# Kernel optimization log

Hardware: AMD Instinct MI355X
Metric: run time of the kernel (lower is better)

## Reference

```python
import jax, jax.numpy as jnp
import numpy as np

E = 768   # embed_size
H = 64    # head_embed_size
B = 8
T = 4096  # == ctx_size


def setup_inputs() -> dict:
    key = jax.random.key(0)
    k1, k2, k3, k4 = jax.random.split(key, 4)
    inputs = jax.random.normal(k1, (B, T, E), dtype=jnp.float32)
    # Linear weights stored as (E, H) so projection is x @ W
    scale = 1.0 / np.sqrt(E)
    Wq = jax.random.uniform(k2, (E, H), dtype=jnp.float32, minval=-scale, maxval=scale)
    Wk = jax.random.uniform(k3, (E, H), dtype=jnp.float32, minval=-scale, maxval=scale)
    Wv = jax.random.uniform(k4, (E, H), dtype=jnp.float32, minval=-scale, maxval=scale)
    return {"inputs": inputs, "Wq": Wq, "Wk": Wk, "Wv": Wv}


def reference(inputs, Wq, Wk, Wv):
    Tlen = inputs.shape[1]
    q = inputs @ Wq  # (B,T,H)
    k = inputs @ Wk  # (B,T,H)
    v = inputs @ Wv  # (B,T,H)
    # NOTE: original module does NOT scale by 1/sqrt(H) — faithful reproduction.
    scores = jnp.einsum('bqh,bkh->bqk', q, k)  # (B,T,T)
    causal = jnp.tril(jnp.ones((Tlen, Tlen), dtype=bool))
    scores = jnp.where(causal, scores, -jnp.inf)
    attn = jax.nn.softmax(scores, axis=-1)
    # dropout=0 -> identity
    out = jnp.einsum('bqk,bkh->bqh', attn, v)  # (B,T,H)
    return out
```

## Files before the change

### kernel.cpp

```cpp
#include <hip/hip_runtime.h>
#include <hip/hip_bf16.h>

#define E_DIM 768
#define H_DIM 64
#define B_SZ 8
#define T_SZ 4096
#define BT (B_SZ * T_SZ)

typedef __attribute__((ext_vector_type(8))) short short8;
typedef __attribute__((ext_vector_type(4))) short bf16x4;
typedef __attribute__((ext_vector_type(4))) float floatx4;

#define RAWBAR() __asm__ volatile("s_waitcnt lgkmcnt(0)\n\ts_barrier" ::: "memory")

static __device__ __forceinline__ unsigned short bf1(float a) {
    __hip_bfloat16 h = __float2bfloat16(a);
    unsigned short u; __builtin_memcpy(&u, &h, 2); return u;
}
static __device__ __forceinline__ unsigned int pk2(float a, float b) {
    __hip_bfloat162 h = __float22bfloat162_rn(float2{a, b});
    unsigned int u; __builtin_memcpy(&u, &h, 4); return u;
}

__global__ __launch_bounds__(256) void prep_w(
    const float* __restrict__ Wq, const float* __restrict__ Wk,
    const float* __restrict__ Wv, unsigned short* __restrict__ Wt)
{
    __shared__ float Ls[64][65];
    const int nt = blockIdx.x;
    const int kc = blockIdx.y;
    const float* __restrict__ W = (nt == 0) ? Wq : (nt == 1) ? Wk : Wv;
    const float scl = (nt == 0) ? 1.44269504088896f : 1.0f;
    const int t = threadIdx.x;
    const int k0 = kc * 64;

#pragma unroll
    for (int it = 0; it < 16; ++it) {
        const int kk = (t >> 6) + it * 4;
        Ls[kk][t & 63] = W[(size_t)(k0 + kk) * H_DIM + (t & 63)];
    }
    __syncthreads();

#pragma unroll
    for (int it = 0; it < 4; ++it) {
        const int nl = (t >> 4) + it * 16;
        const int kl = (t & 15) * 4;
        unsigned int u[2];
        u[0] = pk2(Ls[kl + 0][nl] * scl, Ls[kl + 1][nl] * scl);
        u[1] = pk2(Ls[kl + 2][nl] * scl, Ls[kl + 3][nl] * scl);
        *(uint2*)(Wt + (size_t)(nt * 64 + nl) * E_DIM + k0 + kl) = *(uint2*)u;
    }
}

__global__ __launch_bounds__(768) void proj_mfma(
    const float* __restrict__ X, const unsigned short* __restrict__ Wt,
    unsigned short* __restrict__ Qb, unsigned short* __restrict__ Kb,
    unsigned short* __restrict__ Vtb)
{
    __shared__ unsigned short Xs[2][16][776];

    const int tid  = threadIdx.x;
    const int wave = tid >> 6, lane = tid & 63;
    const int row  = lane & 15, quad = lane >> 4;
    const int m0   = blockIdx.x * 128;

    short8 bfr[24];
    {
        const unsigned short* wp = Wt + (size_t)(wave * 16 + row) * E_DIM + quad * 8;
#pragma unroll
        for (int ks = 0; ks < 24; ++ks) bfr[ks] = *(const short8*)(wp + ks * 32);
    }

    const int srow = tid & 15;
    const int sc   = tid >> 4;
    const float* __restrict__ xbase = X + (size_t)(m0 + srow) * E_DIM + sc * 16;

    float4 fx[4];
#define LDX(mt)                                                               \
    {                                                                         \
        const float* p = xbase + (size_t)(mt) * 16 * E_DIM;                   \
        fx[0] = *(const float4*)(p);     fx[1] = *(const float4*)(p + 4);     \
        fx[2] = *(const float4*)(p + 8); fx[3] = *(const float4*)(p + 12);    \
    }
#define STX(buf)                                                              \
    {                                                                         \
        unsigned int tmp[8];                                                  \
        tmp[0] = pk2(fx[0].x, fx[0].y); tmp[1] = pk2(fx[0].z, fx[0].w);       \
        tmp[2] = pk2(fx[1].x, fx[1].y); tmp[3] = pk2(fx[1].z, fx[1].w);       \
        tmp[4] = pk2(fx[2].x, fx[2].y); tmp[5] = pk2(fx[2].z, fx[2].w);       \
        tmp[6] = pk2(fx[3].x, fx[3].y); tmp[7] = pk2(fx[3].z, fx[3].w);       \
        *(int4*)&Xs[buf][srow][sc * 16]     = *(int4*)&tmp[0];                \
        *(int4*)&Xs[buf][srow][sc * 16 + 8] = *(int4*)&tmp[4];                \
    }

    LDX(0); STX(0); LDX(1);
    RAWBAR();

    const int g  = wave >> 2;
    const int h  = (wave & 3) * 16 + row;
    unsigned short* __restrict__ OQK = (g == 0) ? Qb : Kb;
    const int bb = m0 >> 12;

    int cur = 0;
    for (int mt = 0; mt < 8; ++mt) {
        if (mt < 7) STX(cur ^ 1);
        if (mt < 6) LDX(mt + 2);

        floatx4 a0 = (floatx4)0.0f, a1 = (floatx4)0.0f;
        floatx4 a2 = (floatx4)0.0f, a3 = (floatx4)0.0f;
#pragma unroll
        for (int ks = 0; ks < 6; ++ks) {
            const short8 f0 = *(const short8*)&Xs[cur][row][(ks * 4 + 0) * 32 + quad * 8];
            const short8 f1 = *(const short8*)&Xs[cur][row][(ks * 4 + 1) * 32 + quad * 8];
            const short8 f2 = *(const short8*)&Xs[cur][row][(ks * 4 + 2) * 32 + quad * 8];
            const short8 f3 = *(const short8*)&Xs[cur][row][(ks * 4 + 3) * 32 + quad * 8];
            a0 = __builtin_amdgcn_mfma_f32_16x16x32_bf16(f0, bfr[ks * 4 + 0], a0, 0, 0, 0);
            a1 = __builtin_amdgcn_mfma_f32_16x16x32_bf16(f1, bfr[ks * 4 + 1], a1, 0, 0, 0);
            a2 = __builtin_amdgcn_mfma_f32_16x16x32_bf16(f2, bfr[ks * 4 + 2], a2, 0, 0, 0);
            a3 = __builtin_amdgcn_mfma_f32_16x16x32_bf16(f3, bfr[ks * 4 + 3], a3, 0, 0, 0);
        }
        floatx4 acc;
#pragma unroll
        for (int r = 0; r < 4; ++r) acc[r] = (a0[r] + a1[r]) + (a2[r] + a3[r]);

        const int mr = m0 + mt * 16 + quad * 4;
        if (g < 2) {
#pragma unroll
            for (int r = 0; r < 4; ++r)
                OQK[(size_t)(mr + r) * H_DIM + h] = bf1(acc[r]);
        } else {
            const int t0 = mr & 4095;
            unsigned int u[2];
            u[0] = pk2(acc[0], acc[1]); u[1] = pk2(acc[2], acc[3]);
            *(uint2*)(Vtb + ((size_t)bb * H_DIM + h) * T_SZ + t0) = *(uint2*)u;
        }

        RAWBAR();
        cur ^= 1;
    }
#undef LDX
#undef STX
}

__global__ __launch_bounds__(256, 6) void attn_mfma(
    const unsigned short* __restrict__ Qb,
    const unsigned short* __restrict__ Kb,
    const unsigned short* __restrict__ Vtb,
    float* __restrict__ Opart, float* __restrict__ lpart,
    float* __restrict__ Out)
{
    __shared__ __align__(16) unsigned short KV[2][64][72];
    __shared__ float lc[4][16];

    const int lb = blockIdx.x;
    const int b  = lb & 7;
    const int s  = lb >> 3;
    int qq, c, m;
    if (s < 128)      { m = 4; qq = 96 + (s >> 2); c = s & 3; }
    else if (s < 224) { m = 3; const int t = s - 128; const int t3 = t / 3; qq = 64 + t3; c = t - t3 * 3; }
    else if (s < 288) { m = 2; const int t = s - 224; qq = 32 + (t >> 1); c = t & 1; }
    else              { m = 1; qq = s - 288; c = 0; }
    const int ntot = (qq >> 1) + 1;
    const int k0t  = (c * ntot) / m;
    const int k1t  = ((c + 1) * ntot) / m;
    const int ktd  = ntot - 1;
    const int n    = k1t - k0t;
    const bool split = (m > 1);

    const int tid  = threadIdx.x;
    const int wave = tid >> 6, lane = tid & 63;
    const int col  = lane & 15, quad = lane >> 4;
    const int wq   = wave >> 1;
    const int wk   = wave & 1;

    const size_t base = (size_t)b * T_SZ * H_DIM;
    const int q0  = qq * 32;

    short8 qf0, qf1;
    {
        const unsigned short* qp = Qb + base + (size_t)(q0 + wq * 16 + col) * H_DIM + quad * 8;
        qf0 = *(const short8*)(qp);
        qf1 = *(const short8*)(qp + 32);
    }

    floatx4 o[4];
#pragma unroll
    for (int i = 0; i < 4; ++i) o[i] = (floatx4)0.0f;
    float lp = 0.0f;

    const int krow = tid >> 2, kcol = (tid & 3) * 16;
    const unsigned short* __restrict__ Ksrc = Kb + base + (size_t)krow * H_DIM + kcol;
    const unsigned short* __restrict__ Vsrc = Vtb + ((size_t)b * H_DIM + krow) * T_SZ + kcol;

    int4 kr0, kr1, vr0, vr1;
#define LDKV(t)                                                          \
    {                                                                    \
        const unsigned short* kp = Ksrc + (size_t)(t) * 64 * H_DIM;      \
        kr0 = *(const int4*)kp; kr1 = *(const int4*)(kp + 8);            \
        const unsigned short* vp = Vsrc + (t) * 64;                      \
        vr0 = *(const int4*)vp; vr1 = *(const int4*)(vp + 8);            \
    }
#define STKV()                                                           \
    {                                                                    \
        *(int4*)&KV[0][krow][kcol] = kr0; *(int4*)&KV[0][krow][kcol + 8] = kr1; \
        *(int4*)&KV[1][krow][kcol] = vr0; *(int4*)&KV[1][krow][kcol + 8] = vr1; \
    }

    LDKV(k0t);
    STKV();
    if (n > 1) LDKV(k0t + 1);
    RAWBAR();

    for (int i = 0; i < n; ++i) {
        const int kt = k0t + i;

        floatx4 sv[2];
        __builtin_amdgcn_s_setprio(1);
#pragma unroll
        for (int j = 0; j < 2; ++j) {
            const unsigned short* kp = &KV[0][wk * 32 + j * 16 + col][quad * 8];
            floatx4 a = (floatx4)0.0f;
            a = __builtin_amdgcn_mfma_f32_16x16x32_bf16(*(const short8*)(kp),      qf0, a, 0, 0, 0);
            a = __builtin_amdgcn_mfma_f32_16x16x32_bf16(*(const short8*)(kp + 32), qf1, a, 0, 0, 0);
            sv[j] = a;
        }
        __builtin_amdgcn_s_setprio(0);

        if (kt == ktd) {
            const int qg = q0 + wq * 16 + col;
#pragma unroll
            for (int j = 0; j < 2; ++j) {
                const int kb0 = kt * 64 + wk * 32 + j * 16 + quad * 4;
#pragma unroll
                for (int r = 0; r < 4; ++r)
                    if (kb0 + r > qg) sv[j][r] = -1e30f;
            }
        }

        bf16x4 pa[2];
#pragma unroll
        for (int j = 0; j < 2; ++j) {
            float p0 = exp2f(sv[j][0]);
            float p1 = exp2f(sv[j][1]);
            float p2 = exp2f(sv[j][2]);
            float p3 = exp2f(sv[j][3]);
            lp += (p0 + p1) + (p2 + p3);
            unsigned int u0, u1;
            __asm__("v_cvt_pk_bf16_f32 %0, %1, %2" : "=v"(u0) : "v"(p0), "v"(p1));
            __asm__("v_cvt_pk_bf16_f32 %0, %1, %2" : "=v"(u1) : "v"(p2), "v"(p3));
            union { unsigned int u[2]; bf16x4 v; } pu;
            pu.u[0] = u0; pu.u[1] = u1;
            pa[j] = pu.v;
        }

        __builtin_amdgcn_s_setprio(1);
#pragma unroll
        for (int d = 0; d < 4; ++d) {
#pragma unroll
            for (int j = 0; j < 2; ++j) {
                const bf16x4 vb = *(const bf16x4*)(&KV[1][d * 16 + col][wk * 32 + j * 16 + quad * 4]);
                o[d] = __builtin_amdgcn_mfma_f32_16x16x16bf16_1k(pa[j], vb, o[d], 0, 0, 0);
            }
        }
        __builtin_amdgcn_s_setprio(0);

        RAWBAR();
        if (i + 1 < n) {
            STKV();
            if (i + 2 < n) LDKV(kt + 2);
        }
        RAWBAR();
    }

    lp += __shfl_xor(lp, 16);
    lp += __shfl_xor(lp, 32);
    if (quad == 0) lc[wave][col] = lp;
    __syncthreads();

    float* __restrict__ Oc = (float*)&KV[0][0][0];
#pragma unroll
    for (int r = 0; r < 4; ++r)
#pragma unroll
        for (int d = 0; d < 4; ++d)
            Oc[((wave * 16) + quad * 4 + r) * 64 + d * 16 + col] = o[d][r];
    __syncthreads();

    {
        const int orow = tid >> 3;
        const int d0   = (tid & 7) * 8;
        const int rl   = orow & 15;
        const int wb   = (orow >> 4) * 2;
        const float* p0 = &Oc[((wb * 16) + rl) * 64 + d0];
        const float* p1 = &Oc[(((wb + 1) * 16) + rl) * 64 + d0];
        const float lsum = lc[wb][rl] + lc[wb + 1][rl];
        float4 a0 = *(const float4*)(p0);
        float4 a1 = *(const float4*)(p0 + 4);
        const float4 b0 = *(const float4*)(p1);
        const float4 b1 = *(const float4*)(p1 + 4);
        a0.x += b0.x; a0.y += b0.y; a0.z += b0.z; a0.w += b0.w;
        a1.x += b1.x; a1.y += b1.y; a1.z += b1.z; a1.w += b1.w;
        if (!split) {
            const float inv = 1.0f / lsum;
            a0.x *= inv; a0.y *= inv; a0.z *= inv; a0.w *= inv;
            a1.x *= inv; a1.y *= inv; a1.z *= inv; a1.w *= inv;
            float* op = Out + base + (size_t)(q0 + orow) * H_DIM + d0;
            *(float4*)(op)     = a0;
            *(float4*)(op + 4) = a1;
        } else {
            const int pidx = (b * 96 + (qq - 32)) * 4 + c;
            float* op = Opart + ((size_t)pidx * 32 + orow) * 64 + d0;
            *(float4*)(op)     = a0;
            *(float4*)(op + 4) = a1;
            if ((tid & 7) == 0) lpart[pidx * 32 + orow] = lsum;
        }
    }
#undef LDKV
#undef STKV
}

__global__ __launch_bounds__(256) void attn_combine(
    const float* __restrict__ Opart, const float* __restrict__ lpart,
    float* __restrict__ Out)
{
    const int qi  = blockIdx.x;
    const int b   = blockIdx.y;
    const int qq  = 32 + qi;
    const int m   = (qq < 64) ? 2 : (qq < 96) ? 3 : 4;
    const int tid = threadIdx.x;
    const int orow = tid >> 3;
    const int d0   = (tid & 7) * 8;
    const int p0   = (b * 96 + qi) * 4;

    float4 a0 = {0.f, 0.f, 0.f, 0.f}, a1 = {0.f, 0.f, 0.f, 0.f};
    float l = 0.0f;
    for (int j = 0; j < m; ++j) {
        const float* P = Opart + ((size_t)(p0 + j) * 32 + orow) * 64 + d0;
        const float4 b0 = *(const float4*)(P);
        const float4 b1 = *(const float4*)(P + 4);
        a0.x += b0.x; a0.y += b0.y; a0.z += b0.z; a0.w += b0.w;
        a1.x += b1.x; a1.y += b1.y; a1.z += b1.z; a1.w += b1.w;
        l += lpart[(p0 + j) * 32 + orow];
    }
    const float inv = 1.0f / l;
    a0.x *= inv; a0.y *= inv; a0.z *= inv; a0.w *= inv;
    a1.x *= inv; a1.y *= inv; a1.z *= inv; a1.w *= inv;

    float* op = Out + ((size_t)b * T_SZ + qq * 32 + orow) * H_DIM + d0;
    *(float4*)(op)     = a0;
    *(float4*)(op + 4) = a1;
}

extern "C" void kernel_launch(void* const* d_in, const int* in_sizes, int n_in,
                              void* d_out, int out_size, void* d_ws, size_t ws_size,
                              hipStream_t stream) {
    const float* X  = (const float*)d_in[0];
    const float* Wq = (const float*)d_in[1];
    const float* Wk = (const float*)d_in[2];
    const float* Wv = (const float*)d_in[3];

    unsigned short* Wt  = (unsigned short*)d_ws;
    unsigned short* Qb  = Wt + (size_t)192 * E_DIM;
    unsigned short* Kb  = Qb + (size_t)BT * H_DIM;
    unsigned short* Vtb = Kb + (size_t)BT * H_DIM;
    float* Opart = (float*)(Vtb + (size_t)BT * H_DIM);
    float* lpart = Opart + (size_t)3072 * 32 * 64;

    prep_w<<<dim3(3, 12), 256, 0, stream>>>(Wq, Wk, Wv, Wt);
    proj_mfma<<<256, 768, 0, stream>>>(X, Wt, Qb, Kb, Vtb);
    attn_mfma<<<2560, 256, 0, stream>>>(Qb, Kb, Vtb, Opart, lpart, (float*)d_out);
    attn_combine<<<dim3(96, 8), 256, 0, stream>>>(Opart, lpart, (float*)d_out);
}
```

Baseline: 218.1 us.

## Shrink attention blocks to two waves with 32-key tiles and finer split-K

The attention kernel moves from 4 waves (2 query × 2 key halves) to 2 waves, each owning 16 query rows over a 32-key tile. That removes the cross-wave reduction through shared memory, and each wave writes its output or partial directly. The split-K schedule is rebalanced to up to 6 chunks per 32-row query block, launching 3264 smaller blocks, and the combine kernel is adapted to match. Less shared memory per block and no intra-block reduction should raise occupancy and cut synchronisation. In exchange, each block does less work per barrier, issues more global loads per FLOP, and writes more partials.

```diff
diff --git a/kernel.cpp b/kernel.cpp
--- a/kernel.cpp
+++ b/kernel.cpp
@@ -142,25 +142,27 @@
 #undef STX
 }
 
-__global__ __launch_bounds__(256, 6) void attn_mfma(
+__global__ __launch_bounds__(128, 6) void attn_mfma(
     const unsigned short* __restrict__ Qb,
     const unsigned short* __restrict__ Kb,
     const unsigned short* __restrict__ Vtb,
     float* __restrict__ Opart, float* __restrict__ lpart,
     float* __restrict__ Out)
 {
-    __shared__ __align__(16) unsigned short KV[2][64][72];
-    __shared__ float lc[4][16];
+    __shared__ __align__(16) unsigned short Ks[32][72];
+    __shared__ __align__(16) unsigned short Vs[64][40];
 
     const int lb = blockIdx.x;
     const int b  = lb & 7;
     const int s  = lb >> 3;
     int qq, c, m;
-    if (s < 128)      { m = 4; qq = 96 + (s >> 2); c = s & 3; }
-    else if (s < 224) { m = 3; const int t = s - 128; const int t3 = t / 3; qq = 64 + t3; c = t - t3 * 3; }
-    else if (s < 288) { m = 2; const int t = s - 224; qq = 32 + (t >> 1); c = t & 1; }
-    else              { m = 1; qq = s - 288; c = 0; }
-    const int ntot = (qq >> 1) + 1;
+    if (s < 48)       { m = 6; qq = 127 - s / 6;                      c = s % 6; }
+    else if (s < 168) { m = 5; const int i = s - 48;  qq = 119 - i / 5;  c = i % 5; }
+    else if (s < 264) { m = 4; const int i = s - 168; qq = 95 - (i >> 2); c = i & 3; }
+    else if (s < 336) { m = 3; const int i = s - 264; qq = 71 - i / 3;   c = i % 3; }
+    else if (s < 384) { m = 2; const int i = s - 336; qq = 47 - (i >> 1); c = i & 1; }
+    else              { m = 1; qq = 407 - s; c = 0; }
+    const int ntot = qq + 1;
     const int k0t  = (c * ntot) / m;
     const int k1t  = ((c + 1) * ntot) / m;
     const int ktd  = ntot - 1;
@@ -168,10 +170,9 @@
     const bool split = (m > 1);
 
     const int tid  = threadIdx.x;
-    const int wave = tid >> 6, lane = tid & 63;
+    const int wq   = tid >> 6;
+    const int lane = tid & 63;
     const int col  = lane & 15, quad = lane >> 4;
-    const int wq   = wave >> 1;
-    const int wk   = wave & 1;
 
     const size_t base = (size_t)b * T_SZ * H_DIM;
     const int q0  = qq * 32;
@@ -189,21 +190,22 @@
     float lp = 0.0f;
 
     const int krow = tid >> 2, kcol = (tid & 3) * 16;
+    const int vrow = tid >> 1, vcol = (tid & 1) * 16;
     const unsigned short* __restrict__ Ksrc = Kb + base + (size_t)krow * H_DIM + kcol;
-    const unsigned short* __restrict__ Vsrc = Vtb + ((size_t)b * H_DIM + krow) * T_SZ + kcol;
+    const unsigned short* __restrict__ Vsrc = Vtb + ((size_t)b * H_DIM + vrow) * T_SZ + vcol;
 
     int4 kr0, kr1, vr0, vr1;
 #define LDKV(t)                                                          \
     {                                                                    \
-        const unsigned short* kp = Ksrc + (size_t)(t) * 64 * H_DIM;      \
+        const unsigned short* kp = Ksrc + (size_t)(t) * 32 * H_DIM;      \
         kr0 = *(const int4*)kp; kr1 = *(const int4*)(kp + 8);            \
-        const unsigned short* vp = Vsrc + (t) * 64;                      \
+        const unsigned short* vp = Vsrc + (t) * 32;                      \
         vr0 = *(const int4*)vp; vr1 = *(const int4*)(vp + 8);            \
     }
 #define STKV()                                                           \
     {                                                                    \
-        *(int4*)&KV[0][krow][kcol] = kr0; *(int4*)&KV[0][krow][kcol + 8] = kr1; \
-        *(int4*)&KV[1][krow][kcol] = vr0; *(int4*)&KV[1][krow][kcol + 8] = vr1; \
+        *(int4*)&Ks[krow][kcol] = kr0; *(int4*)&Ks[krow][kcol + 8] = kr1; \
+        *(int4*)&Vs[vrow][vcol] = vr0; *(int4*)&Vs[vrow][vcol + 8] = vr1; \
     }
 
     LDKV(k0t);
@@ -218,7 +220,7 @@
         __builtin_amdgcn_s_setprio(1);
 #pragma unroll
         for (int j = 0; j < 2; ++j) {
-            const unsigned short* kp = &KV[0][wk * 32 + j * 16 + col][quad * 8];
+            const unsigned short* kp = &Ks[j * 16 + col][quad * 8];
             floatx4 a = (floatx4)0.0f;
             a = __builtin_amdgcn_mfma_f32_16x16x32_bf16(*(const short8*)(kp),      qf0, a, 0, 0, 0);
             a = __builtin_amdgcn_mfma_f32_16x16x32_bf16(*(const short8*)(kp + 32), qf1, a, 0, 0, 0);
@@ -230,7 +232,7 @@
             const int qg = q0 + wq * 16 + col;
 #pragma unroll
             for (int j = 0; j < 2; ++j) {
-                const int kb0 = kt * 64 + wk * 32 + j * 16 + quad * 4;
+                const int kb0 = kt * 32 + j * 16 + quad * 4;
 #pragma unroll
                 for (int r = 0; r < 4; ++r)
                     if (kb0 + r > qg) sv[j][r] = -1e30f;
@@ -258,7 +260,7 @@
         for (int d = 0; d < 4; ++d) {
 #pragma unroll
             for (int j = 0; j < 2; ++j) {
-                const bf16x4 vb = *(const bf16x4*)(&KV[1][d * 16 + col][wk * 32 + j * 16 + quad * 4]);
+                const bf16x4 vb = *(const bf16x4*)(&Vs[d * 16 + col][j * 16 + quad * 4]);
                 o[d] = __builtin_amdgcn_mfma_f32_16x16x16bf16_1k(pa[j], vb, o[d], 0, 0, 0);
             }
         }
@@ -274,45 +276,28 @@
 
     lp += __shfl_xor(lp, 16);
     lp += __shfl_xor(lp, 32);
-    if (quad == 0) lc[wave][col] = lp;
-    __syncthreads();
-
-    float* __restrict__ Oc = (float*)&KV[0][0][0];
-#pragma unroll
-    for (int r = 0; r < 4; ++r)
-#pragma unroll
-        for (int d = 0; d < 4; ++d)
-            Oc[((wave * 16) + quad * 4 + r) * 64 + d * 16 + col] = o[d][r];
-    __syncthreads();
-
-    {
-        const int orow = tid >> 3;
-        const int d0   = (tid & 7) * 8;
-        const int rl   = orow & 15;
-        const int wb   = (orow >> 4) * 2;
-        const float* p0 = &Oc[((wb * 16) + rl) * 64 + d0];
-        const float* p1 = &Oc[(((wb + 1) * 16) + rl) * 64 + d0];
-        const float lsum = lc[wb][rl] + lc[wb + 1][rl];
-        float4 a0 = *(const float4*)(p0);
-        float4 a1 = *(const float4*)(p0 + 4);
-        const float4 b0 = *(const float4*)(p1);
-        const float4 b1 = *(const float4*)(p1 + 4);
-        a0.x += b0.x; a0.y += b0.y; a0.z += b0.z; a0.w += b0.w;
-        a1.x += b1.x; a1.y += b1.y; a1.z += b1.z; a1.w += b1.w;
-        if (!split) {
-            const float inv = 1.0f / lsum;
-            a0.x *= inv; a0.y *= inv; a0.z *= inv; a0.w *= inv;
-            a1.x *= inv; a1.y *= inv; a1.z *= inv; a1.w *= inv;
-            float* op = Out + base + (size_t)(q0 + orow) * H_DIM + d0;
-            *(float4*)(op)     = a0;
-            *(float4*)(op + 4) = a1;
-        } else {
-            const int pidx = (b * 96 + (qq - 32)) * 4 + c;
-            float* op = Opart + ((size_t)pidx * 32 + orow) * 64 + d0;
-            *(float4*)(op)     = a0;
-            *(float4*)(op + 4) = a1;
-            if ((tid & 7) == 0) lpart[pidx * 32 + orow] = lsum;
-        }
+    float lr[4];
+#pragma unroll
+    for (int r = 0; r < 4; ++r) lr[r] = __shfl(lp, quad * 4 + r);
+
+    if (!split) {
+        float* op = Out + base + (size_t)(q0 + wq * 16 + quad * 4) * H_DIM;
+#pragma unroll
+        for (int r = 0; r < 4; ++r) {
+            const float inv = 1.0f / lr[r];
+#pragma unroll
+            for (int d = 0; d < 4; ++d)
+                op[(size_t)r * H_DIM + d * 16 + col] = o[d][r] * inv;
+        }
+    } else {
+        const int pidx = (b * 128 + qq) * 6 + c;
+        float* op = Opart + ((size_t)pidx * 32 + wq * 16 + quad * 4) * 64;
+#pragma unroll
+        for (int r = 0; r < 4; ++r)
+#pragma unroll
+            for (int d = 0; d < 4; ++d)
+                op[(size_t)r * 64 + d * 16 + col] = o[d][r];
+        if (quad == 0) lpart[pidx * 32 + wq * 16 + col] = lp;
     }
 #undef LDKV
 #undef STKV
@@ -322,14 +307,13 @@
     const float* __restrict__ Opart, const float* __restrict__ lpart,
     float* __restrict__ Out)
 {
-    const int qi  = blockIdx.x;
+    const int qq  = 24 + blockIdx.x;
     const int b   = blockIdx.y;
-    const int qq  = 32 + qi;
-    const int m   = (qq < 64) ? 2 : (qq < 96) ? 3 : 4;
+    const int m   = (qq + 24) / 24;
     const int tid = threadIdx.x;
     const int orow = tid >> 3;
     const int d0   = (tid & 7) * 8;
-    const int p0   = (b * 96 + qi) * 4;
+    const int p0   = (b * 128 + qq) * 6;
 
     float4 a0 = {0.f, 0.f, 0.f, 0.f}, a1 = {0.f, 0.f, 0.f, 0.f};
     float l = 0.0f;
@@ -363,10 +347,10 @@
     unsigned short* Kb  = Qb + (size_t)BT * H_DIM;
     unsigned short* Vtb = Kb + (size_t)BT * H_DIM;
     float* Opart = (float*)(Vtb + (size_t)BT * H_DIM);
-    float* lpart = Opart + (size_t)3072 * 32 * 64;
+    float* lpart = Opart + (size_t)6144 * 32 * 64;
 
     prep_w<<<dim3(3, 12), 256, 0, stream>>>(Wq, Wk, Wv, Wt);
     proj_mfma<<<256, 768, 0, stream>>>(X, Wt, Qb, Kb, Vtb);
-    attn_mfma<<<2560, 256, 0, stream>>>(Qb, Kb, Vtb, Opart, lpart, (float*)d_out);
-    attn_combine<<<dim3(96, 8), 256, 0, stream>>>(Opart, lpart, (float*)d_out);
-}
+    attn_mfma<<<3264, 128, 0, stream>>>(Qb, Kb, Vtb, Opart, lpart, (float*)d_out);
+    attn_combine<<<dim3(104, 8), 256, 0, stream>>>(Opart, lpart, (float*)d_out);
+}
```

New measurement: 222.8 us. 2.2% more time.

## Permute K rows in LDS so PV uses 16x16x32 MFMA with 8-wide P

Applied to the files above, without the earlier changes.

Stores K tile rows into LDS in a permuted order so each lane's two score fragments cover 8 contiguous keys. The exponentiated probabilities are then packed into one 8-element bf16 vector, and the PV product uses four 16x16x32 MFMAs with 128-bit V loads instead of eight 16x16x16 MFMAs with 64-bit loads. The two QK accumulators are also interleaved so independent MFMAs can overlap. The causal mask indices are updated to match the new key layout; any mistake in the row permutation would silently corrupt results.

```diff
diff --git a/kernel.cpp b/kernel.cpp
--- a/kernel.cpp
+++ b/kernel.cpp
@@ -8,7 +8,6 @@
 #define BT (B_SZ * T_SZ)
 
 typedef __attribute__((ext_vector_type(8))) short short8;
-typedef __attribute__((ext_vector_type(4))) short bf16x4;
 typedef __attribute__((ext_vector_type(4))) float floatx4;
 
 #define RAWBAR() __asm__ volatile("s_waitcnt lgkmcnt(0)\n\ts_barrier" ::: "memory")
@@ -189,6 +188,7 @@
     float lp = 0.0f;
 
     const int krow = tid >> 2, kcol = (tid & 3) * 16;
+    const int kprow = (krow & 32) + ((krow >> 2) & 1) * 16 + ((krow & 31) >> 3) * 4 + (krow & 3);
     const unsigned short* __restrict__ Ksrc = Kb + base + (size_t)krow * H_DIM + kcol;
     const unsigned short* __restrict__ Vsrc = Vtb + ((size_t)b * H_DIM + krow) * T_SZ + kcol;
 
@@ -202,7 +202,7 @@
     }
 #define STKV()                                                           \
     {                                                                    \
-        *(int4*)&KV[0][krow][kcol] = kr0; *(int4*)&KV[0][krow][kcol + 8] = kr1; \
+        *(int4*)&KV[0][kprow][kcol] = kr0; *(int4*)&KV[0][kprow][kcol + 8] = kr1; \
         *(int4*)&KV[1][krow][kcol] = vr0; *(int4*)&KV[1][krow][kcol + 8] = vr1; \
     }
 
@@ -214,53 +214,45 @@
     for (int i = 0; i < n; ++i) {
         const int kt = k0t + i;
 
-        floatx4 sv[2];
+        floatx4 a0 = (floatx4)0.0f, a1 = (floatx4)0.0f;
         __builtin_amdgcn_s_setprio(1);
-#pragma unroll
-        for (int j = 0; j < 2; ++j) {
-            const unsigned short* kp = &KV[0][wk * 32 + j * 16 + col][quad * 8];
-            floatx4 a = (floatx4)0.0f;
-            a = __builtin_amdgcn_mfma_f32_16x16x32_bf16(*(const short8*)(kp),      qf0, a, 0, 0, 0);
-            a = __builtin_amdgcn_mfma_f32_16x16x32_bf16(*(const short8*)(kp + 32), qf1, a, 0, 0, 0);
-            sv[j] = a;
+        {
+            const unsigned short* kp0 = &KV[0][wk * 32 + col][quad * 8];
+            const unsigned short* kp1 = &KV[0][wk * 32 + 16 + col][quad * 8];
+            a0 = __builtin_amdgcn_mfma_f32_16x16x32_bf16(*(const short8*)(kp0),      qf0, a0, 0, 0, 0);
+            a1 = __builtin_amdgcn_mfma_f32_16x16x32_bf16(*(const short8*)(kp1),      qf0, a1, 0, 0, 0);
+            a0 = __builtin_amdgcn_mfma_f32_16x16x32_bf16(*(const short8*)(kp0 + 32), qf1, a0, 0, 0, 0);
+            a1 = __builtin_amdgcn_mfma_f32_16x16x32_bf16(*(const short8*)(kp1 + 32), qf1, a1, 0, 0, 0);
         }
         __builtin_amdgcn_s_setprio(0);
 
         if (kt == ktd) {
             const int qg = q0 + wq * 16 + col;
-#pragma unroll
-            for (int j = 0; j < 2; ++j) {
-                const int kb0 = kt * 64 + wk * 32 + j * 16 + quad * 4;
-#pragma unroll
-                for (int r = 0; r < 4; ++r)
-                    if (kb0 + r > qg) sv[j][r] = -1e30f;
+            const int kb = kt * 64 + wk * 32 + quad * 8;
+#pragma unroll
+            for (int r = 0; r < 4; ++r) {
+                if (kb + r > qg)     a0[r] = -1e30f;
+                if (kb + 4 + r > qg) a1[r] = -1e30f;
             }
         }
 
-        bf16x4 pa[2];
-#pragma unroll
-        for (int j = 0; j < 2; ++j) {
-            float p0 = exp2f(sv[j][0]);
-            float p1 = exp2f(sv[j][1]);
-            float p2 = exp2f(sv[j][2]);
-            float p3 = exp2f(sv[j][3]);
-            lp += (p0 + p1) + (p2 + p3);
-            unsigned int u0, u1;
-            __asm__("v_cvt_pk_bf16_f32 %0, %1, %2" : "=v"(u0) : "v"(p0), "v"(p1));
-            __asm__("v_cvt_pk_bf16_f32 %0, %1, %2" : "=v"(u1) : "v"(p2), "v"(p3));
-            union { unsigned int u[2]; bf16x4 v; } pu;
-            pu.u[0] = u0; pu.u[1] = u1;
-            pa[j] = pu.v;
-        }
+        const float p0 = exp2f(a0[0]), p1 = exp2f(a0[1]), p2 = exp2f(a0[2]), p3 = exp2f(a0[3]);
+        const float p4 = exp2f(a1[0]), p5 = exp2f(a1[1]), p6 = exp2f(a1[2]), p7 = exp2f(a1[3]);
+        lp += ((p0 + p1) + (p2 + p3)) + ((p4 + p5) + (p6 + p7));
+        unsigned int u0, u1, u2, u3;
+        __asm__("v_cvt_pk_bf16_f32 %0, %1, %2" : "=v"(u0) : "v"(p0), "v"(p1));
+        __asm__("v_cvt_pk_bf16_f32 %0, %1, %2" : "=v"(u1) : "v"(p2), "v"(p3));
+        __asm__("v_cvt_pk_bf16_f32 %0, %1, %2" : "=v"(u2) : "v"(p4), "v"(p5));
+        __asm__("v_cvt_pk_bf16_f32 %0, %1, %2" : "=v"(u3) : "v"(p6), "v"(p7));
+        union { unsigned int u[4]; short8 v; } pu;
+        pu.u[0] = u0; pu.u[1] = u1; pu.u[2] = u2; pu.u[3] = u3;
+        const short8 pa = pu.v;
 
         __builtin_amdgcn_s_setprio(1);
 #pragma unroll
         for (int d = 0; d < 4; ++d) {
-#pragma unroll
-            for (int j = 0; j < 2; ++j) {
-                const bf16x4 vb = *(const bf16x4*)(&KV[1][d * 16 + col][wk * 32 + j * 16 + quad * 4]);
-                o[d] = __builtin_amdgcn_mfma_f32_16x16x16bf16_1k(pa[j], vb, o[d], 0, 0, 0);
-            }
+            const short8 vb = *(const short8*)(&KV[1][d * 16 + col][wk * 32 + quad * 8]);
+            o[d] = __builtin_amdgcn_mfma_f32_16x16x32_bf16(pa, vb, o[d], 0, 0, 0);
         }
         __builtin_amdgcn_s_setprio(0);
 
```

Measured after the change: 214.1 us. No clear change (-1.8%).
